# Kernel optimization log

Measured on AMD Instinct MI355X. Metric: run time of the kernel, lower is better.

Reference implementation:

```python
import jax, jax.numpy as jnp
import numpy as np

N_NODES = 131072
N_PER   = 1024     # nodes per graph (equal-sized graphs)
B       = 128      # number of graphs
N_EDGES = 2097152  # avg degree 16
K       = 30       # sort-pool k
HID     = 128
IN_CH   = 14
OUT_DIM = 4


def setup_inputs() -> dict:
    key = jax.random.key(0)
    ks = jax.random.split(key, 20)
    def lin_w(k, out_d, in_d):
        return jax.random.normal(k, (out_d, in_d), jnp.float32) / np.sqrt(in_d)
    x = jax.random.normal(ks[0], (N_NODES, IN_CH), jnp.float32)
    # intra-graph edges: offsets within each graph's contiguous node block
    src_loc = jax.random.randint(ks[1], (N_EDGES,), 0, N_PER)
    dst_loc = jax.random.randint(ks[2], (N_EDGES,), 0, N_PER)
    gid = jnp.repeat(jnp.arange(B), N_EDGES // B) * N_PER
    edge_index = jnp.stack([src_loc + gid, dst_loc + gid]).astype(jnp.int64)
    batch = jnp.repeat(jnp.arange(B), N_PER).astype(jnp.int64)
    return {
        'x': x, 'edge_index': edge_index, 'batch': batch,
        'w_l1': lin_w(ks[3], HID, IN_CH), 'b_l1': jnp.zeros((HID,), jnp.float32),
        'w_r1': lin_w(ks[4], HID, IN_CH),
        'w_l2': lin_w(ks[5], HID, HID),  'b_l2': jnp.zeros((HID,), jnp.float32),
        'w_r2': lin_w(ks[6], HID, HID),
        'w_l3': lin_w(ks[7], HID, HID),  'b_l3': jnp.zeros((HID,), jnp.float32),
        'w_r3': lin_w(ks[8], HID, HID),
        'conv1d_w': jax.random.normal(ks[9], (32, HID, 5), jnp.float32) / np.sqrt(HID * 5),
        'conv1d_b': jnp.zeros((32,), jnp.float32),
        'lin1_w': lin_w(ks[10], HID, 32 * (K - 5 + 1)), 'lin1_b': jnp.zeros((HID,), jnp.float32),
        'lin2_w': lin_w(ks[11], OUT_DIM, HID), 'lin2_b': jnp.zeros((OUT_DIM,), jnp.float32),
    }


def _sage(x, src, dst, deg_inv, w_l, b_l, w_r):
    # PyG SAGEConv (mean aggr): lin_l(mean_{j->i} x_j) + lin_r(x_i)
    agg = jax.ops.segment_sum(x[src], dst, num_segments=N_NODES) * deg_inv
    return agg @ w_l.T + b_l + x @ w_r.T


def reference(x, edge_index, batch,
              w_l1, b_l1, w_r1, w_l2, b_l2, w_r2, w_l3, b_l3, w_r3,
              conv1d_w, conv1d_b, lin1_w, lin1_b, lin2_w, lin2_b):
    src, dst = edge_index[0], edge_index[1]
    deg = jax.ops.segment_sum(jnp.ones((src.shape[0],), jnp.float32), dst,
                              num_segments=N_NODES)
    deg_inv = jnp.where(deg > 0, 1.0 / deg, 0.0)[:, None]

    h = jax.nn.relu(_sage(x, src, dst, deg_inv, w_l1, b_l1, w_r1))
    h = jax.nn.relu(_sage(h, src, dst, deg_inv, w_l2, b_l2, w_r2))
    h = jax.nn.relu(_sage(h, src, dst, deg_inv, w_l3, b_l3, w_r3))

    # global_sort_pool: per-graph sort by last channel (desc), take top-k.
    # Equal-sized graphs with block-structured `batch`, so a reshape suffices
    # (N_PER >= K, hence no fill-value padding in the PyG implementation).
    hb = h.reshape(B, N_PER, HID)
    _, idx = jax.lax.top_k(hb[:, :, -1], K)               # [B, K]
    top = jnp.take_along_axis(hb, idx[:, :, None], axis=1)  # [B, K, HID]

    y = top.transpose(0, 2, 1)                              # [B, HID, K]
    y = jax.lax.conv_general_dilated(y, conv1d_w, (1,), 'VALID',
                                     dimension_numbers=('NCH', 'OIH', 'NCH'))
    y = jax.nn.relu(y + conv1d_b[None, :, None])            # [B, 32, K-4]
    y = y.reshape(B, -1)                                    # [B, 832]
    y = jax.nn.relu(y @ lin1_w.T + lin1_b)
    # dropout p=0.5 is inference-time identity
    return y @ lin2_w.T + lin2_b
```

## Files before the change

### kernel.cpp

```cpp
#include <hip/hip_runtime.h>
#include <hip/hip_bf16.h>
#include <hip/hip_fp16.h>

#define N_NODES 131072
#define N_PER   1024
#define NGRAPH  128
#define N_EDGES 2097152
#define EPG     16384
#define KSP     30
#define HID     128
#define IN_CH   14
#define OUT_DIM 4

typedef __attribute__((ext_vector_type(8))) short    v8s;
typedef __attribute__((ext_vector_type(8))) _Float16 v8h;
typedef __attribute__((ext_vector_type(4))) float    v4f;

__device__ inline v8h as_h(v8s s){ union { v8s s; v8h h; } u; u.s = s; return u.h; }

#define LOSCALE 4096.0f
#define INV_LOSCALE (1.0f/4096.0f)
__device__ inline void f2split(float v, ushort& hi, ushort& lo){
  float av = fabsf(v);
  __half h = (av < 6.103515625e-05f) ? __ushort_as_half((ushort)0) : __float2half(v);
  hi = __half_as_ushort(h);
  lo = __half_as_ushort(__float2half((v - __half2float(h)) * LOSCALE));
}
__device__ inline float f2join(ushort hi, ushort lo){
  return __half2float(__ushort_as_half(hi)) + __half2float(__ushort_as_half(lo)) * INV_LOSCALE;
}

__global__ __launch_bounds__(1024) void k_csr(const int* __restrict__ src, const int* __restrict__ dst,
    ushort* __restrict__ csr, int* __restrict__ row_ptr, float* __restrict__ dinv){
  __shared__ ushort lcsr[EPG];
  __shared__ int ldeg[N_PER];
  __shared__ int lrp[N_PER];
  __shared__ int lcur[N_PER];
  int g = blockIdx.x, t = threadIdx.x;
  int base = g*EPG;
  ldeg[t] = 0;
  __syncthreads();
  #pragma unroll
  for (int r = 0; r < EPG/1024; ++r)
    atomicAdd(&ldeg[dst[base + r*1024 + t] & (N_PER-1)], 1);
  __syncthreads();
  int d = ldeg[t];
  lrp[t] = d;
  __syncthreads();
  for (int ofs = 1; ofs < N_PER; ofs <<= 1){
    int v = lrp[t];
    int add = (t >= ofs) ? lrp[t-ofs] : 0;
    __syncthreads();
    lrp[t] = v + add;
    __syncthreads();
  }
  int ex = lrp[t] - d;
  lcur[t] = ex;
  row_ptr[g*N_PER + t] = base + ex;
  dinv[g*N_PER + t] = d > 0 ? 1.0f/(float)d : 0.0f;
  if (g == NGRAPH-1 && t == 0) row_ptr[N_NODES] = N_EDGES;
  __syncthreads();
  #pragma unroll
  for (int r = 0; r < EPG/1024; ++r){
    int e = base + r*1024 + t;
    int dl = dst[e] & (N_PER-1);
    int pos = atomicAdd(&lcur[dl], 1);
    lcsr[pos] = (ushort)(src[e] & (N_PER-1));
  }
  __syncthreads();
  uint* gout = (uint*)(csr + base);
  const uint* lin = (const uint*)lcsr;
  #pragma unroll
  for (int r = 0; r < EPG/2048; ++r)
    gout[r*1024 + t] = lin[r*1024 + t];
}

__global__ __launch_bounds__(256) void k_pack_x(const float* __restrict__ x,
                                                ushort* __restrict__ xhi, ushort* __restrict__ xlo){
  int i = blockIdx.x*256 + threadIdx.x;
  int n = i >> 5, k = i & 31;
  float v = (k < IN_CH) ? x[n*IN_CH + k] : 0.0f;
  int dst = (n >> 4)*512 + ((k >> 3)*16 + (n & 15))*8 + (k & 7);
  ushort hi, lo; f2split(v, hi, lo);
  xhi[dst] = hi; xlo[dst] = lo;
}

__global__ __launch_bounds__(256) void k_pack_w(const float* __restrict__ wl, const float* __restrict__ wr,
    ushort* __restrict__ wlh, ushort* __restrict__ wll,
    ushort* __restrict__ wrh, ushort* __restrict__ wrl, int KC, int kin){
  int i = blockIdx.x*256 + threadIdx.x;
  int Kp = KC*32;
  if (i >= 256*Kp) return;
  int which = i / (128*Kp);
  int r = (i / Kp) & 127;
  int k = i % Kp;
  const float* w = which ? wr : wl;
  float v = (k < kin) ? w[r*kin + k] : 0.0f;
  ushort hi, lo; f2split(v, hi, lo);
  int dst = ((r >> 4)*KC + (k >> 5))*512 + ((((k & 31) >> 3))*16 + (r & 15))*8 + (k & 7);
  if (which){ wrh[dst] = hi; wrl[dst] = lo; }
  else      { wlh[dst] = hi; wll[dst] = lo; }
}

__global__ __launch_bounds__(256) void k_transpose_cw(const float* __restrict__ cw, float* __restrict__ cwT){
  int e = blockIdx.x*256 + threadIdx.x;
  if (e < 32*HID*5){
    int o = e / 640, rem = e % 640;
    cwT[rem*32 + o] = cw[e];
  }
}

#define FXS 262144.0f
__global__ __launch_bounds__(1024) void k_gather(
    const ushort* __restrict__ Hhi, const ushort* __restrict__ Hlo,
    ushort* __restrict__ Mhi, ushort* __restrict__ Mlo,
    const int* __restrict__ row_ptr, const ushort* __restrict__ csr,
    const float* __restrict__ dinv, int KC){
  __shared__ int ldsI[N_PER*20];
  int P = KC*2;
  int g = blockIdx.x / P, p = blockIdx.x % P;
  int kc = p >> 1, half = p & 1;
  int t = threadIdx.x;
  for (int it = t; it < 16384; it += 1024){
    int Tl = it >> 8, e = it & 255;
    int idx = (((g*64 + Tl)*KC + kc) << 9) + (half << 8) + e;
    float v = f2join(Hhi[idx], Hlo[idx]);
    int l = e >> 3, j = e & 7;
    int m = l & 15, qh = l >> 4;
    ldsI[(Tl*16 + m)*20 + qh*8 + j] = __float2int_rn(v*FXS);
  }
  __syncthreads();
  int o2 = t & 1, ns = t >> 1;
  #pragma unroll
  for (int rep = 0; rep < 2; ++rep){
    int n = ns + rep*512;
    int node = g*N_PER + n;
    int s = row_ptr[node], e = row_ptr[node+1];
    int a0=0,a1=0,a2=0,a3=0,a4=0,a5=0,a6=0,a7=0;
    int j2 = s;
    for (; j2 + 2 <= e; j2 += 2){
      int la = csr[j2];
      int lb = csr[j2+1];
      const int4* ra = (const int4*)&ldsI[la*20 + o2*8];
      const int4* rb = (const int4*)&ldsI[lb*20 + o2*8];
      int4 x0 = ra[0], x1 = ra[1], y0 = rb[0], y1 = rb[1];
      a0 += x0.x + y0.x; a1 += x0.y + y0.y; a2 += x0.z + y0.z; a3 += x0.w + y0.w;
      a4 += x1.x + y1.x; a5 += x1.y + y1.y; a6 += x1.z + y1.z; a7 += x1.w + y1.w;
    }
    if (j2 < e){
      int la = csr[j2];
      const int4* ra = (const int4*)&ldsI[la*20 + o2*8];
      int4 x0 = ra[0], x1 = ra[1];
      a0 += x0.x; a1 += x0.y; a2 += x0.z; a3 += x0.w;
      a4 += x1.x; a5 += x1.y; a6 += x1.z; a7 += x1.w;
    }
    float di = dinv[node] * (1.0f/FXS);
    float mv[8] = {(float)a0*di,(float)a1*di,(float)a2*di,(float)a3*di,
                   (float)a4*di,(float)a5*di,(float)a6*di,(float)a7*di};
    int q = half*2 + o2;
    int base = (((g*64 + (n >> 4))*KC + kc) << 9) + (q*16 + (n & 15))*8;
    ushort hs[8], ls[8];
    #pragma unroll
    for (int ii = 0; ii < 8; ++ii) f2split(mv[ii], hs[ii], ls[ii]);
    *(ushort4*)&Mhi[base]   = make_ushort4(hs[0],hs[1],hs[2],hs[3]);
    *(ushort4*)&Mhi[base+4] = make_ushort4(hs[4],hs[5],hs[6],hs[7]);
    *(ushort4*)&Mlo[base]   = make_ushort4(ls[0],ls[1],ls[2],ls[3]);
    *(ushort4*)&Mlo[base+4] = make_ushort4(ls[4],ls[5],ls[6],ls[7]);
  }
}

template<int KCI, int MODE>
__global__ __launch_bounds__(256, 2) void k_gemm(
    const ushort* __restrict__ Ah1, const ushort* __restrict__ Al1,
    const ushort* __restrict__ Ah2, const ushort* __restrict__ Al2,
    const ushort* __restrict__ wlh, const ushort* __restrict__ wll,
    const ushort* __restrict__ wrh, const ushort* __restrict__ wrl,
    const float* __restrict__ bias, ushort* Hho, ushort* Hlo2, float* key){
  __shared__ ushort smB[4*8*512];
  int t = threadIdx.x, w = t >> 6, l = t & 63;
  int q = l >> 4, m = l & 15;
  int rtl = (w & 1)*2;
  int ctb = (w >> 1)*4;
  int t0 = blockIdx.x*4;
  const ushort* warr[4] = {wlh, wll, wrh, wrl};
  v4f acc1[2][4], acc2[2][4];
  #pragma unroll
  for (int a = 0; a < 2; ++a)
    #pragma unroll
    for (int b = 0; b < 4; ++b){ acc1[a][b] = (v4f){0.f,0.f,0.f,0.f}; acc2[a][b] = (v4f){0.f,0.f,0.f,0.f}; }
  v8s* smv = (v8s*)smB;
  v8s pre[8];
  #pragma unroll
  for (int i2 = 0; i2 < 8; ++i2){
    int i = i2*256 + t; int r = i >> 9, e2 = i & 511, ct = e2 >> 6, j = e2 & 63;
    pre[i2] = *(const v8s*)(warr[r] + ((ct*KCI + 0) << 9) + j*8);
  }
  #pragma unroll
  for (int i2 = 0; i2 < 8; ++i2) smv[i2*256 + t] = pre[i2];

  for (int kc = 0; kc < KCI; ++kc){
    __syncthreads();
    if (kc + 1 < KCI){
      #pragma unroll
      for (int i2 = 0; i2 < 8; ++i2){
        int i = i2*256 + t; int r = i >> 9, e2 = i & 511, ct = e2 >> 6, j = e2 & 63;
        pre[i2] = *(const v8s*)(warr[r] + ((ct*KCI + kc + 1) << 9) + j*8);
      }
    }
    v8h a1h[2], a1l[2], a2h[2], a2l[2];
    #pragma unroll
    for (int rr = 0; rr < 2; ++rr){
      int aoff = (((t0 + rtl + rr)*KCI + kc) << 9) + l*8;
      a1h[rr] = as_h(*(const v8s*)(Ah1 + aoff));
      a1l[rr] = as_h(*(const v8s*)(Al1 + aoff));
      a2h[rr] = as_h(*(const v8s*)(Ah2 + aoff));
      a2l[rr] = as_h(*(const v8s*)(Al2 + aoff));
    }
    #pragma unroll
    for (int cc = 0; cc < 4; ++cc){
      int ct = ctb + cc;
      v8h b0h = as_h(smv[(0*8 + ct)*64 + l]);
      v8h b0l = as_h(smv[(1*8 + ct)*64 + l]);
      v8h b1h = as_h(smv[(2*8 + ct)*64 + l]);
      v8h b1l = as_h(smv[(3*8 + ct)*64 + l]);
      #pragma unroll
      for (int rr = 0; rr < 2; ++rr){
        acc1[rr][cc] = __builtin_amdgcn_mfma_f32_16x16x32_f16(a1h[rr], b0h, acc1[rr][cc], 0, 0, 0);
        acc2[rr][cc] = __builtin_amdgcn_mfma_f32_16x16x32_f16(a1l[rr], b0h, acc2[rr][cc], 0, 0, 0);
        acc2[rr][cc] = __builtin_amdgcn_mfma_f32_16x16x32_f16(a1h[rr], b0l, acc2[rr][cc], 0, 0, 0);
        acc1[rr][cc] = __builtin_amdgcn_mfma_f32_16x16x32_f16(a2h[rr], b1h, acc1[rr][cc], 0, 0, 0);
        acc2[rr][cc] = __builtin_amdgcn_mfma_f32_16x16x32_f16(a2l[rr], b1h, acc2[rr][cc], 0, 0, 0);
        acc2[rr][cc] = __builtin_amdgcn_mfma_f32_16x16x32_f16(a2h[rr], b1l, acc2[rr][cc], 0, 0, 0);
      }
    }
    __syncthreads();
    if (kc + 1 < KCI){
      #pragma unroll
      for (int i2 = 0; i2 < 8; ++i2) smv[i2*256 + t] = pre[i2];
    }
  }
  #pragma unroll
  for (int cc = 0; cc < 4; ++cc){
    int ct_g = ctb + cc;
    float badd = bias[ct_g*16 + m];
    #pragma unroll
    for (int rr = 0; rr < 2; ++rr){
      int T = t0 + rtl + rr;
      #pragma unroll
      for (int r = 0; r < 4; ++r){
        float v = fmaxf(acc1[rr][cc][r] + acc2[rr][cc][r]*INV_LOSCALE + badd, 0.0f);
        int lane2 = ((ct_g & 1)*2 + (m >> 3))*16 + q*4 + r;
        int didx = ((T*4 + (ct_g >> 1)) << 9) + lane2*8 + (m & 7);
        if (MODE == 0){
          ushort hi, lo; f2split(v, hi, lo);
          Hho[didx] = hi; Hlo2[didx] = lo;
        } else {
          Hho[didx] = __half_as_ushort(__float2half(v));
          if (ct_g == 7 && m == 15) key[T*16 + q*4 + r] = v;
        }
      }
    }
  }
}

__global__ __launch_bounds__(1024) void k_sortpool(const float* __restrict__ keyv, int* __restrict__ sel){
  int g = blockIdx.x, t = threadIdx.x;
  __shared__ unsigned long long key[N_PER];
  __shared__ unsigned long long wred[16];
  float v = keyv[g*N_PER + t];
  key[t] = (((unsigned long long)__float_as_uint(v)) << 10) | (unsigned long long)(N_PER-1 - t);
  __syncthreads();
  for (int r = 0; r < KSP; ++r){
    unsigned long long k = key[t];
    #pragma unroll
    for (int ofs = 32; ofs > 0; ofs >>= 1){
      unsigned long long o2 = __shfl_down(k, ofs, 64);
      if (o2 > k) k = o2;
    }
    if ((t & 63) == 0) wred[t >> 6] = k;
    __syncthreads();
    if (t == 0){
      unsigned long long mm = wred[0];
      #pragma unroll
      for (int j = 1; j < 16; ++j) if (wred[j] > mm) mm = wred[j];
      int idx = (N_PER-1) - (int)(mm & 1023ULL);
      sel[g*KSP + r] = idx;
      key[idx] = 0ULL;
    }
    __syncthreads();
  }
}

__global__ __launch_bounds__(256) void k_head(const ushort* __restrict__ Hhi, const int* __restrict__ sel,
    const float* __restrict__ cwT, const float* __restrict__ cb,
    const float* __restrict__ l1w, const float* __restrict__ l1b,
    const float* __restrict__ l2w, const float* __restrict__ l2b,
    float* __restrict__ out){
  __shared__ __align__(16) float toplds[KSP*HID];
  __shared__ float ypart[8][832];
  __shared__ __align__(16) float yv[832];
  __shared__ float zv[HID];
  int g = blockIdx.x, t = threadIdx.x;
  for (int e = t; e < KSP*HID; e += 256){
    int tt = e >> 7, c = e & 127;
    int n = g*N_PER + sel[g*KSP + tt];
    int idx = ((n >> 4)*4 + (c >> 5))*512 + (((c & 31) >> 3)*16 + (n & 15))*8 + (c & 7);
    toplds[e] = __half2float(__ushort_as_half(Hhi[idx]));
  }
  __syncthreads();
  int o = t & 31, cch = t >> 5;
  float acc[26];
  #pragma unroll
  for (int th = 0; th < 26; ++th) acc[th] = 0.0f;
  for (int c = cch*16; c < cch*16 + 16; ++c){
    float tcol[KSP];
    #pragma unroll
    for (int tt = 0; tt < KSP; ++tt) tcol[tt] = toplds[tt*HID + c];
    float w5[5];
    #pragma unroll
    for (int s = 0; s < 5; ++s) w5[s] = cwT[(c*5 + s)*32 + o];
    #pragma unroll
    for (int th = 0; th < 26; ++th){
      float a2 = acc[th];
      #pragma unroll
      for (int s = 0; s < 5; ++s) a2 += tcol[th + s]*w5[s];
      acc[th] = a2;
    }
  }
  #pragma unroll
  for (int th = 0; th < 26; ++th) ypart[cch][o*26 + th] = acc[th];
  __syncthreads();
  for (int idx = t; idx < 832; idx += 256){
    float s2 = 0.0f;
    #pragma unroll
    for (int j = 0; j < 8; ++j) s2 += ypart[j][idx];
    yv[idx] = fmaxf(s2 + cb[idx / 26], 0.0f);
  }
  __syncthreads();
  if (t < HID){
    float a3 = l1b[t];
    const float4* wr4 = (const float4*)&l1w[t*832];
    const float4* yr4 = (const float4*)yv;
    #pragma unroll 4
    for (int k = 0; k < 208; ++k){
      float4 wv = wr4[k]; float4 yq = yr4[k];
      a3 += wv.x*yq.x + wv.y*yq.y + wv.z*yq.z + wv.w*yq.w;
    }
    zv[t] = fmaxf(a3, 0.0f);
  }
  __syncthreads();
  if (t < OUT_DIM){
    float a4 = l2b[t];
    for (int j = 0; j < HID; ++j) a4 += zv[j]*l2w[t*HID + j];
    out[g*OUT_DIM + t] = a4;
  }
}

extern "C" void kernel_launch(void* const* d_in, const int* in_sizes, int n_in,
                              void* d_out, int out_size, void* d_ws, size_t ws_size,
                              hipStream_t stream){
  const float* x   = (const float*)d_in[0];
  const int*   ei  = (const int*)d_in[1];
  const float* wl1 = (const float*)d_in[3];
  const float* b1  = (const float*)d_in[4];
  const float* wr1 = (const float*)d_in[5];
  const float* wl2 = (const float*)d_in[6];
  const float* b2  = (const float*)d_in[7];
  const float* wr2 = (const float*)d_in[8];
  const float* wl3 = (const float*)d_in[9];
  const float* b3  = (const float*)d_in[10];
  const float* wr3 = (const float*)d_in[11];
  const float* cw  = (const float*)d_in[12];
  const float* cb  = (const float*)d_in[13];
  const float* l1w = (const float*)d_in[14];
  const float* l1b = (const float*)d_in[15];
  const float* l2w = (const float*)d_in[16];
  const float* l2b = (const float*)d_in[17];
  float* out = (float*)d_out;
  const int* esrc = ei;
  const int* edst = ei + N_EDGES;

  char* p = (char*)d_ws;
  auto alloc = [&](size_t bytes)->char*{ char* r = p; p += (bytes + 255) & ~(size_t)255; return r; };
  int*    row_ptr = (int*)alloc((size_t)(N_NODES+1)*4);
  float*  dinv    = (float*)alloc((size_t)N_NODES*4);
  ushort* csr     = (ushort*)alloc((size_t)N_EDGES*2);
  int*    sel     = (int*)alloc((size_t)NGRAPH*KSP*4);
  float*  cwT     = (float*)alloc((size_t)32*HID*5*4);
  float*  keyv    = (float*)alloc((size_t)N_NODES*4);
  ushort* Xhi     = (ushort*)alloc((size_t)N_NODES*32*2);
  ushort* Xlo     = (ushort*)alloc((size_t)N_NODES*32*2);
  ushort* Mhi     = (ushort*)alloc((size_t)N_NODES*HID*2);
  ushort* Mlo     = (ushort*)alloc((size_t)N_NODES*HID*2);
  ushort* Hhi     = (ushort*)alloc((size_t)N_NODES*HID*2);
  ushort* Hlo     = (ushort*)alloc((size_t)N_NODES*HID*2);
  ushort* w1lh = (ushort*)alloc(512*8*2);  ushort* w1ll = (ushort*)alloc(512*8*2);
  ushort* w1rh = (ushort*)alloc(512*8*2);  ushort* w1rl = (ushort*)alloc(512*8*2);
  ushort* w2lh = (ushort*)alloc(512*32*2); ushort* w2ll = (ushort*)alloc(512*32*2);
  ushort* w2rh = (ushort*)alloc(512*32*2); ushort* w2rl = (ushort*)alloc(512*32*2);
  ushort* w3lh = (ushort*)alloc(512*32*2); ushort* w3ll = (ushort*)alloc(512*32*2);
  ushort* w3rh = (ushort*)alloc(512*32*2); ushort* w3rl = (ushort*)alloc(512*32*2);

  k_csr<<<NGRAPH, 1024, 0, stream>>>(esrc, edst, csr, row_ptr, dinv);

  k_pack_x<<<(N_NODES*32)/256, 256, 0, stream>>>(x, Xhi, Xlo);
  k_pack_w<<<(256*32)/256, 256, 0, stream>>>(wl1, wr1, w1lh, w1ll, w1rh, w1rl, 1, IN_CH);
  k_pack_w<<<(256*128)/256, 256, 0, stream>>>(wl2, wr2, w2lh, w2ll, w2rh, w2rl, 4, 128);
  k_pack_w<<<(256*128)/256, 256, 0, stream>>>(wl3, wr3, w3lh, w3ll, w3rh, w3rl, 4, 128);
  k_transpose_cw<<<(32*HID*5 + 255)/256, 256, 0, stream>>>(cw, cwT);

  const int GB = N_NODES/64;

  k_gather<<<NGRAPH*2, 1024, 0, stream>>>(Xhi, Xlo, Mhi, Mlo, row_ptr, csr, dinv, 1);
  k_gemm<1,0><<<GB, 256, 0, stream>>>(Mhi, Mlo, Xhi, Xlo,
      w1lh, w1ll, w1rh, w1rl, b1, Hhi, Hlo, nullptr);
  k_gather<<<NGRAPH*8, 1024, 0, stream>>>(Hhi, Hlo, Mhi, Mlo, row_ptr, csr, dinv, 4);
  k_gemm<4,0><<<GB, 256, 0, stream>>>(Mhi, Mlo, Hhi, Hlo,
      w2lh, w2ll, w2rh, w2rl, b2, Hhi, Hlo, nullptr);
  k_gather<<<NGRAPH*8, 1024, 0, stream>>>(Hhi, Hlo, Mhi, Mlo, row_ptr, csr, dinv, 4);
  k_gemm<4,1><<<GB, 256, 0, stream>>>(Mhi, Mlo, Hhi, Hlo,
      w3lh, w3ll, w3rh, w3rl, b3, Hhi, nullptr, keyv);

  k_sortpool<<<NGRAPH, 1024, 0, stream>>>(keyv, sel);
  k_head<<<NGRAPH, 256, 0, stream>>>(Hhi, sel, cwT, cb, l1w, l1b, l2w, l2b, out);
}
```

Measured before the change: 410.5 us.

## Pad CSR rows to multiples of eight and vectorize gather index loads

The CSR builder pads each node's neighbor list to a multiple of 8 entries, filled with a dummy index pointing to an all-zero LDS row. It stores indices pre-scaled by the LDS row stride and records per-node padded counts. The gather loop loads 8 indices with one 128-bit load and accumulates 8 neighbors per iteration with no tail handling. This cuts index-load count and loop overhead, at the cost of extra LDS reads for padding entries and a larger CSR buffer.

Result: slower. 620.0 us (+51.0%).

```diff
diff --git a/kernel.cpp b/kernel.cpp
--- a/kernel.cpp
+++ b/kernel.cpp
@@ -7,6 +7,8 @@
 #define NGRAPH  128
 #define N_EDGES 2097152
 #define EPG     16384
+#define PADE    24576
+#define LSTR    20
 #define KSP     30
 #define HID     128
 #define IN_CH   14
@@ -31,21 +33,25 @@
 }
 
 __global__ __launch_bounds__(1024) void k_csr(const int* __restrict__ src, const int* __restrict__ dst,
-    ushort* __restrict__ csr, int* __restrict__ row_ptr, float* __restrict__ dinv){
-  __shared__ ushort lcsr[EPG];
+    ushort* __restrict__ csr, int* __restrict__ row_ptr, ushort* __restrict__ pcnt,
+    float* __restrict__ dinv){
+  __shared__ ushort lcsr[PADE];
   __shared__ int ldeg[N_PER];
   __shared__ int lrp[N_PER];
   __shared__ int lcur[N_PER];
   int g = blockIdx.x, t = threadIdx.x;
   int base = g*EPG;
   ldeg[t] = 0;
+  #pragma unroll
+  for (int r = 0; r < PADE/1024; ++r) lcsr[r*1024 + t] = (ushort)(1024*LSTR);
   __syncthreads();
   #pragma unroll
   for (int r = 0; r < EPG/1024; ++r)
     atomicAdd(&ldeg[dst[base + r*1024 + t] & (N_PER-1)], 1);
   __syncthreads();
   int d = ldeg[t];
-  lrp[t] = d;
+  int pd = (d + 7) & ~7;
+  lrp[t] = pd;
   __syncthreads();
   for (int ofs = 1; ofs < N_PER; ofs <<= 1){
     int v = lrp[t];
@@ -54,24 +60,24 @@
     lrp[t] = v + add;
     __syncthreads();
   }
-  int ex = lrp[t] - d;
+  int ex = lrp[t] - pd;
   lcur[t] = ex;
-  row_ptr[g*N_PER + t] = base + ex;
+  row_ptr[g*N_PER + t] = g*PADE + ex;
+  pcnt[g*N_PER + t] = (ushort)pd;
   dinv[g*N_PER + t] = d > 0 ? 1.0f/(float)d : 0.0f;
-  if (g == NGRAPH-1 && t == 0) row_ptr[N_NODES] = N_EDGES;
   __syncthreads();
   #pragma unroll
   for (int r = 0; r < EPG/1024; ++r){
     int e = base + r*1024 + t;
     int dl = dst[e] & (N_PER-1);
     int pos = atomicAdd(&lcur[dl], 1);
-    lcsr[pos] = (ushort)(src[e] & (N_PER-1));
-  }
-  __syncthreads();
-  uint* gout = (uint*)(csr + base);
+    lcsr[pos] = (ushort)((src[e] & (N_PER-1)) * LSTR);
+  }
+  __syncthreads();
+  uint* gout = (uint*)(csr + (size_t)g*PADE);
   const uint* lin = (const uint*)lcsr;
   #pragma unroll
-  for (int r = 0; r < EPG/2048; ++r)
+  for (int r = 0; r < PADE/2048; ++r)
     gout[r*1024 + t] = lin[r*1024 + t];
 }
 
@@ -114,9 +120,9 @@
 __global__ __launch_bounds__(1024) void k_gather(
     const ushort* __restrict__ Hhi, const ushort* __restrict__ Hlo,
     ushort* __restrict__ Mhi, ushort* __restrict__ Mlo,
-    const int* __restrict__ row_ptr, const ushort* __restrict__ csr,
-    const float* __restrict__ dinv, int KC){
-  __shared__ int ldsI[N_PER*20];
+    const int* __restrict__ row_ptr, const ushort* __restrict__ pcnt,
+    const ushort* __restrict__ csr, const float* __restrict__ dinv, int KC){
+  __shared__ int ldsI[(N_PER+1)*LSTR];
   int P = KC*2;
   int g = blockIdx.x / P, p = blockIdx.x % P;
   int kc = p >> 1, half = p & 1;
@@ -127,32 +133,42 @@
     float v = f2join(Hhi[idx], Hlo[idx]);
     int l = e >> 3, j = e & 7;
     int m = l & 15, qh = l >> 4;
-    ldsI[(Tl*16 + m)*20 + qh*8 + j] = __float2int_rn(v*FXS);
-  }
+    ldsI[(Tl*16 + m)*LSTR + qh*8 + j] = __float2int_rn(v*FXS);
+  }
+  if (t < LSTR) ldsI[N_PER*LSTR + t] = 0;
   __syncthreads();
   int o2 = t & 1, ns = t >> 1;
   #pragma unroll
   for (int rep = 0; rep < 2; ++rep){
     int n = ns + rep*512;
     int node = g*N_PER + n;
-    int s = row_ptr[node], e = row_ptr[node+1];
+    int s = row_ptr[node];
+    int cnt = pcnt[node];
+    const uint4* c4 = (const uint4*)(csr + s);
+    int ob = o2*8;
     int a0=0,a1=0,a2=0,a3=0,a4=0,a5=0,a6=0,a7=0;
-    int j2 = s;
-    for (; j2 + 2 <= e; j2 += 2){
-      int la = csr[j2];
-      int lb = csr[j2+1];
-      const int4* ra = (const int4*)&ldsI[la*20 + o2*8];
-      const int4* rb = (const int4*)&ldsI[lb*20 + o2*8];
-      int4 x0 = ra[0], x1 = ra[1], y0 = rb[0], y1 = rb[1];
-      a0 += x0.x + y0.x; a1 += x0.y + y0.y; a2 += x0.z + y0.z; a3 += x0.w + y0.w;
-      a4 += x1.x + y1.x; a5 += x1.y + y1.y; a6 += x1.z + y1.z; a7 += x1.w + y1.w;
-    }
-    if (j2 < e){
-      int la = csr[j2];
-      const int4* ra = (const int4*)&ldsI[la*20 + o2*8];
-      int4 x0 = ra[0], x1 = ra[1];
-      a0 += x0.x; a1 += x0.y; a2 += x0.z; a3 += x0.w;
-      a4 += x1.x; a5 += x1.y; a6 += x1.z; a7 += x1.w;
+    for (int c = 0; c < cnt; c += 8){
+      uint4 v = c4[c >> 3];
+      int e0 = (int)(v.x & 0xFFFFu) + ob, e1 = (int)(v.x >> 16) + ob;
+      int e2 = (int)(v.y & 0xFFFFu) + ob, e3 = (int)(v.y >> 16) + ob;
+      int e4 = (int)(v.z & 0xFFFFu) + ob, e5 = (int)(v.z >> 16) + ob;
+      int e6 = (int)(v.w & 0xFFFFu) + ob, e7 = (int)(v.w >> 16) + ob;
+      int4 x0 = *(const int4*)&ldsI[e0], x1 = *(const int4*)&ldsI[e0+4];
+      int4 y0 = *(const int4*)&ldsI[e1], y1 = *(const int4*)&ldsI[e1+4];
+      int4 z0 = *(const int4*)&ldsI[e2], z1 = *(const int4*)&ldsI[e2+4];
+      int4 u0 = *(const int4*)&ldsI[e3], u1 = *(const int4*)&ldsI[e3+4];
+      a0 += x0.x + y0.x + z0.x + u0.x;  a1 += x0.y + y0.y + z0.y + u0.y;
+      a2 += x0.z + y0.z + z0.z + u0.z;  a3 += x0.w + y0.w + z0.w + u0.w;
+      a4 += x1.x + y1.x + z1.x + u1.x;  a5 += x1.y + y1.y + z1.y + u1.y;
+      a6 += x1.z + y1.z + z1.z + u1.z;  a7 += x1.w + y1.w + z1.w + u1.w;
+      x0 = *(const int4*)&ldsI[e4]; x1 = *(const int4*)&ldsI[e4+4];
+      y0 = *(const int4*)&ldsI[e5]; y1 = *(const int4*)&ldsI[e5+4];
+      z0 = *(const int4*)&ldsI[e6]; z1 = *(const int4*)&ldsI[e6+4];
+      u0 = *(const int4*)&ldsI[e7]; u1 = *(const int4*)&ldsI[e7+4];
+      a0 += x0.x + y0.x + z0.x + u0.x;  a1 += x0.y + y0.y + z0.y + u0.y;
+      a2 += x0.z + y0.z + z0.z + u0.z;  a3 += x0.w + y0.w + z0.w + u0.w;
+      a4 += x1.x + y1.x + z1.x + u1.x;  a5 += x1.y + y1.y + z1.y + u1.y;
+      a6 += x1.z + y1.z + z1.z + u1.z;  a7 += x1.w + y1.w + z1.w + u1.w;
     }
     float di = dinv[node] * (1.0f/FXS);
     float mv[8] = {(float)a0*di,(float)a1*di,(float)a2*di,(float)a3*di,
@@ -382,9 +398,10 @@
 
   char* p = (char*)d_ws;
   auto alloc = [&](size_t bytes)->char*{ char* r = p; p += (bytes + 255) & ~(size_t)255; return r; };
-  int*    row_ptr = (int*)alloc((size_t)(N_NODES+1)*4);
+  int*    row_ptr = (int*)alloc((size_t)N_NODES*4);
+  ushort* pcnt    = (ushort*)alloc((size_t)N_NODES*2);
   float*  dinv    = (float*)alloc((size_t)N_NODES*4);
-  ushort* csr     = (ushort*)alloc((size_t)N_EDGES*2);
+  ushort* csr     = (ushort*)alloc((size_t)NGRAPH*PADE*2);
   int*    sel     = (int*)alloc((size_t)NGRAPH*KSP*4);
   float*  cwT     = (float*)alloc((size_t)32*HID*5*4);
   float*  keyv    = (float*)alloc((size_t)N_NODES*4);
@@ -401,7 +418,7 @@
   ushort* w3lh = (ushort*)alloc(512*32*2); ushort* w3ll = (ushort*)alloc(512*32*2);
   ushort* w3rh = (ushort*)alloc(512*32*2); ushort* w3rl = (ushort*)alloc(512*32*2);
 
-  k_csr<<<NGRAPH, 1024, 0, stream>>>(esrc, edst, csr, row_ptr, dinv);
+  k_csr<<<NGRAPH, 1024, 0, stream>>>(esrc, edst, csr, row_ptr, pcnt, dinv);
 
   k_pack_x<<<(N_NODES*32)/256, 256, 0, stream>>>(x, Xhi, Xlo);
   k_pack_w<<<(256*32)/256, 256, 0, stream>>>(wl1, wr1, w1lh, w1ll, w1rh, w1rl, 1, IN_CH);
@@ -411,13 +428,13 @@
 
   const int GB = N_NODES/64;
 
-  k_gather<<<NGRAPH*2, 1024, 0, stream>>>(Xhi, Xlo, Mhi, Mlo, row_ptr, csr, dinv, 1);
+  k_gather<<<NGRAPH*2, 1024, 0, stream>>>(Xhi, Xlo, Mhi, Mlo, row_ptr, pcnt, csr, dinv, 1);
   k_gemm<1,0><<<GB, 256, 0, stream>>>(Mhi, Mlo, Xhi, Xlo,
       w1lh, w1ll, w1rh, w1rl, b1, Hhi, Hlo, nullptr);
-  k_gather<<<NGRAPH*8, 1024, 0, stream>>>(Hhi, Hlo, Mhi, Mlo, row_ptr, csr, dinv, 4);
+  k_gather<<<NGRAPH*8, 1024, 0, stream>>>(Hhi, Hlo, Mhi, Mlo, row_ptr, pcnt, csr, dinv, 4);
   k_gemm<4,0><<<GB, 256, 0, stream>>>(Mhi, Mlo, Hhi, Hlo,
       w2lh, w2ll, w2rh, w2rl, b2, Hhi, Hlo, nullptr);
-  k_gather<<<NGRAPH*8, 1024, 0, stream>>>(Hhi, Hlo, Mhi, Mlo, row_ptr, csr, dinv, 4);
+  k_gather<<<NGRAPH*8, 1024, 0, stream>>>(Hhi, Hlo, Mhi, Mlo, row_ptr, pcnt, csr, dinv, 4);
   k_gemm<4,1><<<GB, 256, 0, stream>>>(Mhi, Mlo, Hhi, Hlo,
       w3lh, w3ll, w3rh, w3rl, b3, Hhi, nullptr, keyv);
 
```
